# Optimization experiments

Hardware: AMD Instinct MI355X
Metric: run time of the kernel (lower is better)

The kernel has to match this reference:

```python
import jax, jax.numpy as jnp
import numpy as np

DIM = 256
HEADS = 8
DIM_HEAD = 64
HIDDEN = HEADS * DIM_HEAD
SCALE = DIM_HEAD ** -0.5


def setup_inputs() -> dict:
    key = jax.random.key(0)
    ks = jax.random.split(key, 8)
    std = 0.02
    x = jax.random.normal(ks[0], (2, DIM, 16, 64, 64), dtype=jnp.float32)
    Wq = jax.random.normal(ks[1], (HIDDEN, DIM), dtype=jnp.float32) * std
    Wk = jax.random.normal(ks[2], (HIDDEN, DIM), dtype=jnp.float32) * std
    Wv = jax.random.normal(ks[3], (HIDDEN, DIM), dtype=jnp.float32) * std
    Wg = jax.random.normal(ks[4], (HIDDEN, DIM), dtype=jnp.float32) * std
    bg = jnp.zeros((HIDDEN,), dtype=jnp.float32)
    Wo = jax.random.normal(ks[5], (DIM, HIDDEN), dtype=jnp.float32) * std
    bo = jnp.zeros((DIM,), dtype=jnp.float32)
    return {"x": x, "Wq": Wq, "Wk": Wk, "Wv": Wv, "Wg": Wg, "bg": bg, "Wo": Wo, "bo": bo}


def _proj(x, W):  # 1x1 conv, no bias: (B,C,H,W) @ (O,C) -> (B,O,H,W)
    return jnp.einsum('bchw,oc->bohw', x, W)


def reference(x, Wq, Wk, Wv, Wg, bg, Wo, bo):
    b, c, f, h, w = x.shape
    xf = x.transpose(0, 2, 1, 3, 4).reshape(b * f, c, h, w)  # (bf, c, h, w)
    q = _proj(xf, Wq)
    k = _proj(xf, Wk)
    v = _proj(xf, Wv)
    g = _proj(xf, Wg) + bg[None, :, None, None]
    # softmax over height for q, width for k (pre-reshape, as in torch)
    q = jax.nn.softmax(q, axis=-2)
    k = jax.nn.softmax(k, axis=-1)

    def to_heads(t):  # (bf, H*D, h, w) -> (bf, H, h*w, D)
        return t.reshape(b * f, HEADS, DIM_HEAD, h * w).transpose(0, 1, 3, 2)

    q, k, v, g = map(to_heads, (q, k, v, g))
    q = jax.nn.elu(q) + 1.0
    k = jax.nn.elu(k) + 1.0
    g = jax.nn.sigmoid(g)

    kv = jnp.einsum('bhnd,bhne->bhde', k, v)
    k_sum = k.sum(axis=2)                                   # (bf, H, D)
    z = 1.0 / jnp.maximum(jnp.einsum('bhnd,bhd->bhn', q, k_sum), 1e-6)
    out = jnp.einsum('bhnd,bhde->bhne', q * SCALE, kv)
    out = out * z[..., None] * g                            # (bf, H, n, D)

    out = out.transpose(0, 1, 3, 2).reshape(b * f, HIDDEN, h, w)
    out = jnp.einsum('bchw,oc->bohw', out, Wo) + bo[None, :, None, None]
    return out.reshape(b, f, c, h, w).transpose(0, 2, 1, 3, 4)
```

## Files before the change

kernel.cpp:

```cpp
#include <hip/hip_runtime.h>


typedef unsigned short u16;
typedef unsigned int u32;
typedef __bf16 bf16x8 __attribute__((ext_vector_type(8)));
typedef float f32x4 __attribute__((ext_vector_type(4)));

__device__ inline float bf2f(u16 v) { union { u32 i; float f; } u; u.i = ((u32)v) << 16; return u.f; }
__device__ inline u16 f2bf(float f) {
    union { float f; u32 i; } u; u.f = f;
    u32 r = (u.i + 0x7fffu + ((u.i >> 16) & 1u)) >> 16;
    return (u16)r;
}
__device__ inline void split2(float v, u16& h, u16& l) {
    h = f2bf(v);
    l = f2bf(v - bf2f(h));
}

__global__ void k_cvt_w(const float* __restrict__ Wq, const float* __restrict__ Wk,
                        const float* __restrict__ Wv, const float* __restrict__ Wg,
                        const float* __restrict__ Wo,
                        u16* __restrict__ Wh, u16* __restrict__ Wl,
                        u16* __restrict__ Woh, u16* __restrict__ Wol)
{
    int idx = blockIdx.x * 256 + threadIdx.x;
    if (idx < 524288) {
        int o = idx >> 8, c = idx & 255;
        int which = o >> 9, r = o & 511;
        const float* s = (which == 0) ? Wq : (which == 1) ? Wk : (which == 2) ? Wv : Wg;
        u16 h, l; split2(s[r * 256 + c], h, l);
        Wh[idx] = h; Wl[idx] = l;
    } else {
        int j = idx - 524288;
        if (j < 131072) { u16 h, l; split2(Wo[j], h, l); Woh[j] = h; Wol[j] = l; }
    }
}

__global__ __launch_bounds__(256) void k_cvt_x(const float* __restrict__ x,
                                               u16* __restrict__ xh, u16* __restrict__ xl,
                                               int c0)
{
    __shared__ __align__(16) u16 tileh[64 * 132];
    __shared__ __align__(16) u16 tilel[64 * 132];
    const int t = threadIdx.x;
    const int bfl = blockIdx.y;
    const int bfg = c0 + bfl;
    const int n0 = blockIdx.x * 128;
    const int b_ = bfg >> 4, f_ = bfg & 15;
    for (int s = 0; s < 2; ++s) {
        for (int ch2 = 0; ch2 < 2; ++ch2) {
            __syncthreads();
            for (int p = 0; p < 8; ++p) {
                int cl = p * 16 + (t >> 4);
                int c = ch2 * 128 + cl;
                const float* sp = x + (((size_t)b_ * 256 + c) * 16 + f_) * 4096
                                    + n0 + s * 64 + (t & 15) * 4;
                float4 v = *(const float4*)sp;
                float vv[4] = { v.x, v.y, v.z, v.w };
#pragma unroll
                for (int j = 0; j < 4; ++j) {
                    int nl = (t & 15) * 4 + j;
                    u16 h, l; split2(vv[j], h, l);
                    tileh[nl * 132 + cl] = h;
                    tilel[nl * 132 + cl] = l;
                }
            }
            __syncthreads();
#pragma unroll
            for (int i = 0; i < 4; ++i) {
                int flat = t + i * 256;
                int nn = flat >> 4, cc = flat & 15;
                size_t off = ((size_t)bfl * 4096 + n0 + s * 64 + nn) * 256 + ch2 * 128 + cc * 8;
                *(uint4*)(xh + off) = *(const uint4*)(tileh + nn * 132 + cc * 8);
                *(uint4*)(xl + off) = *(const uint4*)(tilel + nn * 132 + cc * 8);
            }
        }
    }
}

__global__ __launch_bounds__(256) void k_proj(
    const u16* __restrict__ Wh, const u16* __restrict__ Wl,
    const u16* __restrict__ xh, const u16* __restrict__ xl,
    const float* __restrict__ bg,
    u16* __restrict__ kh, u16* __restrict__ kl,
    u16* __restrict__ vh, u16* __restrict__ vl,
    float* __restrict__ qf, float* __restrict__ gf, int pass)
{
    __shared__ __align__(16) char smem[65536];
    u16* Ah = (u16*)smem;
    u16* Al = (u16*)(smem + 16384);
    u16* Bh = (u16*)(smem + 32768);
    u16* Bl = (u16*)(smem + 49152);
    float* Csh = (float*)smem;
    const int t = threadIdx.x;
    const int bfl = blockIdx.z;
    const int by = blockIdx.y;
    const int m0 = (pass == 0) ? (512 + by * 128)
                               : ((by < 4) ? by * 128 : 1536 + (by - 4) * 128);
    const int n0 = blockIdx.x * 128;
    const int lane = t & 63, wv = t >> 6, wm = wv >> 1, wn = wv & 1;
    f32x4 acc[4][4] = {};
    const u16* Aph = Wh + (size_t)m0 * 256;
    const u16* Apl = Wl + (size_t)m0 * 256;
    const u16* Bph = xh + ((size_t)bfl * 4096 + n0) * 256;
    const u16* Bpl = xl + ((size_t)bfl * 4096 + n0) * 256;
    const int srow = t >> 3, sci = t & 7;

    for (int kt = 0; kt < 4; ++kt) {
        const int k0 = kt * 64;
#pragma unroll
        for (int p = 0; p < 4; ++p) {
            int row = srow + p * 32;
            size_t go = (size_t)row * 256 + k0 + sci * 8;
            int sc = (sci ^ (row & 7)) * 8;
            *(uint4*)(Ah + row * 64 + sc) = *(const uint4*)(Aph + go);
            *(uint4*)(Al + row * 64 + sc) = *(const uint4*)(Apl + go);
            *(uint4*)(Bh + row * 64 + sc) = *(const uint4*)(Bph + go);
            *(uint4*)(Bl + row * 64 + sc) = *(const uint4*)(Bpl + go);
        }
        __syncthreads();
#pragma unroll
        for (int kk = 0; kk < 2; ++kk) {
            bf16x8 afh[4], afl[4], bfh[4], bfl_[4];
#pragma unroll
            for (int i = 0; i < 4; ++i) {
                int ra = wm * 64 + i * 16 + (lane & 15);
                int ca = ((kk * 4 + (lane >> 4)) ^ (ra & 7)) * 8;
                afh[i] = *(const bf16x8*)(Ah + ra * 64 + ca);
                afl[i] = *(const bf16x8*)(Al + ra * 64 + ca);
                int rb = wn * 64 + i * 16 + (lane & 15);
                int cb = ((kk * 4 + (lane >> 4)) ^ (rb & 7)) * 8;
                bfh[i] = *(const bf16x8*)(Bh + rb * 64 + cb);
                bfl_[i] = *(const bf16x8*)(Bl + rb * 64 + cb);
            }
#pragma unroll
            for (int mi = 0; mi < 4; ++mi)
#pragma unroll
                for (int ni = 0; ni < 4; ++ni) {
                    acc[mi][ni] = __builtin_amdgcn_mfma_f32_16x16x32_bf16(afh[mi], bfh[ni], acc[mi][ni], 0, 0, 0);
                    acc[mi][ni] = __builtin_amdgcn_mfma_f32_16x16x32_bf16(afh[mi], bfl_[ni], acc[mi][ni], 0, 0, 0);
                    acc[mi][ni] = __builtin_amdgcn_mfma_f32_16x16x32_bf16(afl[mi], bfh[ni], acc[mi][ni], 0, 0, 0);
                }
        }
        __syncthreads();
    }

    const int sector = m0 >> 9;
    for (int ph = 0; ph < 2; ++ph) {
        if (wn == ph) {
#pragma unroll
            for (int mi = 0; mi < 4; ++mi)
#pragma unroll
                for (int ni = 0; ni < 4; ++ni)
#pragma unroll
                    for (int r = 0; r < 4; ++r) {
                        int gr = wm * 64 + mi * 16 + (lane >> 4) * 4 + r;
                        int gcl = ni * 16 + (lane & 15);
                        Csh[gr * 69 + gcl] = acc[mi][ni][r];
                    }
        }
        __syncthreads();
        if (t < 128) {
            const float* src = Csh + t * 69;
            const int oloc = (m0 & 511) + t;
            const size_t doff = ((size_t)bfl * 512 + oloc) * 4096 + n0 + ph * 64;
            if (sector == 0) {
#pragma unroll
                for (int i = 0; i < 16; ++i) {
                    float4 o = { src[i * 4], src[i * 4 + 1], src[i * 4 + 2], src[i * 4 + 3] };
                    *(float4*)(qf + doff + i * 4) = o;
                }
            } else if (sector == 2) {
#pragma unroll
                for (int i = 0; i < 8; ++i) {
                    union { u16 h[8]; uint4 u; } ph_, pl_;
#pragma unroll
                    for (int j = 0; j < 8; ++j) split2(src[i * 8 + j], ph_.h[j], pl_.h[j]);
                    *(uint4*)(vh + doff + i * 8) = ph_.u;
                    *(uint4*)(vl + doff + i * 8) = pl_.u;
                }
            } else if (sector == 1) {
                float mx = -3.0e38f;
                for (int j = 0; j < 64; ++j) mx = fmaxf(mx, src[j]);
                float sum = 0.f;
                for (int j = 0; j < 64; ++j) sum += expf(src[j] - mx);
                float rs = 1.0f / sum;
#pragma unroll
                for (int i = 0; i < 8; ++i) {
                    union { u16 h[8]; uint4 u; } ph_, pl_;
#pragma unroll
                    for (int j = 0; j < 8; ++j) {
                        float p = expf(src[i * 8 + j] - mx) * rs;
                        split2(p, ph_.h[j], pl_.h[j]);
                    }
                    *(uint4*)(kh + doff + i * 8) = ph_.u;
                    *(uint4*)(kl + doff + i * 8) = pl_.u;
                }
            } else {
                float bgv = bg[oloc];
#pragma unroll
                for (int i = 0; i < 16; ++i) {
                    float4 o;
                    float* po = (float*)&o;
#pragma unroll
                    for (int j = 0; j < 4; ++j)
                        po[j] = 1.0f / (1.0f + expf(-(src[i * 4 + j] + bgv)));
                    *(float4*)(gf + doff + i * 4) = o;
                }
            }
        }
        __syncthreads();
    }
}

__global__ __launch_bounds__(256) void k_smq(float* __restrict__ qf)
{
    __shared__ float img[64 * 65];
    __shared__ float red[256];
    __shared__ float mxv[64];
    __shared__ float smv[64];
    const int t = threadIdx.x;
    float* base = qf + ((size_t)blockIdx.y * 512 + blockIdx.x) * 4096;
#pragma unroll
    for (int i = 0; i < 16; ++i) {
        int n = t + i * 256;
        img[(n >> 6) * 65 + (n & 63)] = base[n];
    }
    __syncthreads();
    const int part = t >> 6, wc = t & 63;
    float mx = -3.0e38f;
    for (int hh = 0; hh < 16; ++hh) mx = fmaxf(mx, img[(part * 16 + hh) * 65 + wc]);
    red[t] = mx;
    __syncthreads();
    if (t < 64) mxv[t] = fmaxf(fmaxf(red[t], red[64 + t]), fmaxf(red[128 + t], red[192 + t]));
    __syncthreads();
    float m = mxv[wc], s = 0.f;
    for (int hh = 0; hh < 16; ++hh) s += expf(img[(part * 16 + hh) * 65 + wc] - m);
    red[t] = s;
    __syncthreads();
    if (t < 64) smv[t] = red[t] + red[64 + t] + red[128 + t] + red[192 + t];
    __syncthreads();
    float rm = mxv[t & 63], rs = 1.0f / smv[t & 63];
#pragma unroll
    for (int i = 0; i < 16; ++i) {
        int n = t + i * 256;
        base[n] = expf(img[(n >> 6) * 65 + (n & 63)] - rm) * rs;
    }
}

__global__ __launch_bounds__(512) void k_kv(
    const u16* __restrict__ kh, const u16* __restrict__ kl,
    const u16* __restrict__ vh, const u16* __restrict__ vl,
    float* __restrict__ kvp, float* __restrict__ ksp)
{
    __shared__ float kvl[4096];
    __shared__ float redv[512];
    __shared__ float redk[512];
    __shared__ float vsum[64];
    const int t = threadIdx.x;
    const int qq = blockIdx.x;
    const int bh = blockIdx.y;
    const int NBH = gridDim.y;
    const size_t hb = (size_t)bh * 64 * 4096;
    const u16* bkh = kh + hb;
    const u16* bkl = kl + hb;
    const u16* bvh = vh + hb;
    const u16* bvl = vl + hb;
#pragma unroll
    for (int i = 0; i < 8; ++i) kvl[t + i * 512] = 0.f;
    __syncthreads();
    const int lane = t & 63, wv = t >> 6;
    f32x4 acc[4][4] = {};
    for (int it = 0; it < 4; ++it) {
        int n = qq * 1024 + wv * 128 + it * 32 + (lane >> 4) * 8;
        bf16x8 ah[4], al[4], bh_[4], bl_[4];
#pragma unroll
        for (int i = 0; i < 4; ++i) {
            size_t ro = (size_t)(i * 16 + (lane & 15)) * 4096 + n;
            ah[i]  = *(const bf16x8*)(bkh + ro);
            al[i]  = *(const bf16x8*)(bkl + ro);
            bh_[i] = *(const bf16x8*)(bvh + ro);
            bl_[i] = *(const bf16x8*)(bvl + ro);
        }
#pragma unroll
        for (int di = 0; di < 4; ++di)
#pragma unroll
            for (int ei = 0; ei < 4; ++ei) {
                acc[di][ei] = __builtin_amdgcn_mfma_f32_16x16x32_bf16(ah[di], bh_[ei], acc[di][ei], 0, 0, 0);
                acc[di][ei] = __builtin_amdgcn_mfma_f32_16x16x32_bf16(ah[di], bl_[ei], acc[di][ei], 0, 0, 0);
                acc[di][ei] = __builtin_amdgcn_mfma_f32_16x16x32_bf16(al[di], bh_[ei], acc[di][ei], 0, 0, 0);
            }
    }
#pragma unroll
    for (int di = 0; di < 4; ++di)
#pragma unroll
        for (int ei = 0; ei < 4; ++ei)
#pragma unroll
            for (int r = 0; r < 4; ++r) {
                int d = di * 16 + (lane >> 4) * 4 + r;
                int e = ei * 16 + (lane & 15);
                atomicAdd(&kvl[d * 64 + e], acc[di][ei][r]);
            }
    const int e = t & 63, part = t >> 6;
    float sv = 0.f, sk = 0.f;
    const size_t so = (size_t)e * 4096 + qq * 1024 + part * 128;
    for (int i = 0; i < 16; ++i) {
        union { uint4 v; u16 h[8]; } a1, a2, b1, b2;
        a1.v = *(const uint4*)(bvh + so + i * 8);
        a2.v = *(const uint4*)(bvl + so + i * 8);
        b1.v = *(const uint4*)(bkh + so + i * 8);
        b2.v = *(const uint4*)(bkl + so + i * 8);
#pragma unroll
        for (int j = 0; j < 8; ++j) {
            sv += bf2f(a1.h[j]) + bf2f(a2.h[j]);
            sk += bf2f(b1.h[j]) + bf2f(b2.h[j]);
        }
    }
    redv[t] = sv; redk[t] = sk;
    __syncthreads();
    if (t < 64) {
        float a = 0.f, b = 0.f;
#pragma unroll
        for (int p = 0; p < 8; ++p) { a += redv[p * 64 + t]; b += redk[p * 64 + t]; }
        vsum[t] = a;
        ksp[((size_t)qq * NBH + bh) * 64 + t] = 1024.0f + b;
    }
    __syncthreads();
    float* outp = kvp + ((size_t)qq * NBH + bh) * 4096;
#pragma unroll
    for (int i = 0; i < 8; ++i) {
        int idx = t + i * 512;
        outp[idx] = kvl[idx] + vsum[idx & 63];
    }
}

__global__ __launch_bounds__(256) void k_att(
    const float* __restrict__ qf, const float* __restrict__ gf,
    const float* __restrict__ kvp, const float* __restrict__ ksp,
    u16* __restrict__ atth, u16* __restrict__ attl, int NBH)
{
    __shared__ __align__(16) float sh[4352 + 64 + 64 + 16];
    float* kvl = sh;
    float* ksl = sh + 4352;
    float* csl = sh + 4416;
    float* kstp = sh + 4480;
    const int t = threadIdx.x;
    const int bh = blockIdx.z * 8 + blockIdx.y;
#pragma unroll
    for (int i = 0; i < 16; ++i) {
        int idx = t + i * 256;
        float s = 0.f;
#pragma unroll
        for (int q = 0; q < 4; ++q) s += kvp[((size_t)q * NBH + bh) * 4096 + idx];
        kvl[(idx >> 6) * 68 + (idx & 63)] = s;
    }
    if (t < 64) {
        float s = 0.f;
#pragma unroll
        for (int q = 0; q < 4; ++q) s += ksp[((size_t)q * NBH + bh) * 64 + t];
        ksl[t] = s;
    }
    __syncthreads();
    if (t < 64) {
        float s = 0.f;
        for (int d = 0; d < 64; ++d) s += kvl[d * 68 + t];
        csl[t] = s;
    }
    if (t == 64) {
        float s = 0.f;
        for (int d = 0; d < 64; ++d) s += ksl[d];
        kstp[0] = s;
    }
    __syncthreads();
    const int n = blockIdx.x * 256 + t;
    const float* qp = qf + ((size_t)bh * 64) * 4096 + n;
    f32x4 sa[16];
#pragma unroll
    for (int i = 0; i < 16; ++i) sa[i] = *(const f32x4*)&csl[i * 4];
    float sz = kstp[0];
    for (int d = 0; d < 64; ++d) {
        float pq = qp[(size_t)d * 4096];
        sz += pq * ksl[d];
        const f32x4* kr = (const f32x4*)&kvl[d * 68];
#pragma unroll
        for (int i = 0; i < 16; ++i) sa[i] += pq * kr[i];
    }
    float zz = 0.125f / fmaxf(sz, 1e-6f);
    const float* gp = gf + ((size_t)bh * 64) * 4096 + n;
    const size_t ab = (((size_t)(bh >> 3)) * 4096 + n) * 512 + (bh & 7) * 64;
#pragma unroll
    for (int eo = 0; eo < 8; ++eo) {
        union { u16 h[8]; uint4 u; } ph_, pl_;
#pragma unroll
        for (int j = 0; j < 8; ++j) {
            int e = eo * 8 + j;
            float val = sa[e >> 2][e & 3] * zz * gp[(size_t)e * 4096];
            split2(val, ph_.h[j], pl_.h[j]);
        }
        *(uint4*)(atth + ab + eo * 8) = ph_.u;
        *(uint4*)(attl + ab + eo * 8) = pl_.u;
    }
}

__global__ __launch_bounds__(256) void k_out(
    const u16* __restrict__ Woh, const u16* __restrict__ Wol,
    const u16* __restrict__ atth, const u16* __restrict__ attl,
    const float* __restrict__ bo, float* __restrict__ out, int c0)
{
    __shared__ __align__(16) u16 smem[32768];
    u16* Ah = smem;
    u16* Al = smem + 8192;
    u16* Bh = smem + 16384;
    u16* Bl = smem + 24576;
    const int t = threadIdx.x;
    const int bfl = blockIdx.z;
    const int bfg = c0 + bfl;
    const int m0 = blockIdx.y * 128;
    const int n0 = blockIdx.x * 128;
    const int lane = t & 63, wv = t >> 6, wm = wv >> 1, wn = wv & 1;
    f32x4 acc[4][4] = {};
    const u16* Aph = Woh + (size_t)m0 * 512;
    const u16* Apl = Wol + (size_t)m0 * 512;
    const u16* Bph = atth + ((size_t)bfl * 4096 + n0) * 512;
    const u16* Bpl = attl + ((size_t)bfl * 4096 + n0) * 512;
    const int srow = t >> 3, sci = t & 7;
    for (int kt = 0; kt < 8; ++kt) {
        const int k0 = kt * 64;
#pragma unroll
        for (int p = 0; p < 4; ++p) {
            int row = srow + p * 32;
            size_t go = (size_t)row * 512 + k0 + sci * 8;
            int sc = (sci ^ (row & 7)) * 8;
            *(uint4*)(Ah + row * 64 + sc) = *(const uint4*)(Aph + go);
            *(uint4*)(Al + row * 64 + sc) = *(const uint4*)(Apl + go);
            *(uint4*)(Bh + row * 64 + sc) = *(const uint4*)(Bph + go);
            *(uint4*)(Bl + row * 64 + sc) = *(const uint4*)(Bpl + go);
        }
        __syncthreads();
#pragma unroll
        for (int kk = 0; kk < 2; ++kk) {
            bf16x8 afh[4], afl[4], bfh[4], bfl_[4];
#pragma unroll
            for (int i = 0; i < 4; ++i) {
                int ra = wm * 64 + i * 16 + (lane & 15);
                int ca = ((kk * 4 + (lane >> 4)) ^ (ra & 7)) * 8;
                afh[i] = *(const bf16x8*)(Ah + ra * 64 + ca);
                afl[i] = *(const bf16x8*)(Al + ra * 64 + ca);
                int rb = wn * 64 + i * 16 + (lane & 15);
                int cb = ((kk * 4 + (lane >> 4)) ^ (rb & 7)) * 8;
                bfh[i] = *(const bf16x8*)(Bh + rb * 64 + cb);
                bfl_[i] = *(const bf16x8*)(Bl + rb * 64 + cb);
            }
#pragma unroll
            for (int mi = 0; mi < 4; ++mi)
#pragma unroll
                for (int ni = 0; ni < 4; ++ni) {
                    acc[mi][ni] = __builtin_amdgcn_mfma_f32_16x16x32_bf16(afh[mi], bfh[ni], acc[mi][ni], 0, 0, 0);
                    acc[mi][ni] = __builtin_amdgcn_mfma_f32_16x16x32_bf16(afh[mi], bfl_[ni], acc[mi][ni], 0, 0, 0);
                    acc[mi][ni] = __builtin_amdgcn_mfma_f32_16x16x32_bf16(afl[mi], bfh[ni], acc[mi][ni], 0, 0, 0);
                }
        }
        __syncthreads();
    }
    const int b_ = bfg >> 4, f_ = bfg & 15;
#pragma unroll
    for (int mi = 0; mi < 4; ++mi)
#pragma unroll
        for (int ni = 0; ni < 4; ++ni)
#pragma unroll
            for (int r = 0; r < 4; ++r) {
                int o = m0 + wm * 64 + mi * 16 + (lane >> 4) * 4 + r;
                int nn = n0 + wn * 64 + ni * 16 + (lane & 15);
                out[(((size_t)b_ * 256 + o) * 16 + f_) * 4096 + nn] = acc[mi][ni][r] + bo[o];
            }
}

extern "C" void kernel_launch(void* const* d_in, const int* in_sizes, int n_in,
                              void* d_out, int out_size, void* d_ws, size_t ws_size,
                              hipStream_t stream)
{
    const float* x  = (const float*)d_in[0];
    const float* Wq = (const float*)d_in[1];
    const float* Wk = (const float*)d_in[2];
    const float* Wv = (const float*)d_in[3];
    const float* Wg = (const float*)d_in[4];
    const float* bg = (const float*)d_in[5];
    const float* Wo = (const float*)d_in[6];
    const float* bo = (const float*)d_in[7];
    float* out = (float*)d_out;
    char* ws = (char*)d_ws;

    const size_t PER_BF = 29892608ull;
    const size_t FIXED  = 2621440ull;
    int CH = 32;
    while (CH > 1 && FIXED + (size_t)CH * PER_BF > ws_size) CH >>= 1;
    const int nch = 32 / CH;

    u16* Wh  = (u16*)(ws);
    u16* Wl  = (u16*)(ws + 1048576);
    u16* Woh = (u16*)(ws + 2097152);
    u16* Wol = (u16*)(ws + 2359296);
    char* dyn = ws + FIXED;
    u16*   xh   = (u16*)(dyn);
    u16*   xl   = (u16*)(dyn + (size_t)CH * 2097152);
    u16*   kh   = (u16*)(dyn + (size_t)CH * 4194304);
    u16*   kl   = (u16*)(dyn + (size_t)CH * 8388608);
    u16*   vh   = (u16*)(dyn + (size_t)CH * 12582912);
    u16*   vl   = (u16*)(dyn + (size_t)CH * 16777216);
    u16*   atth = (u16*)(dyn + (size_t)CH * 20971520);
    u16*   attl = (u16*)(dyn + (size_t)CH * 25165824);
    float* kvp  = (float*)(dyn + (size_t)CH * 29360128);
    float* ksp  = (float*)(dyn + (size_t)CH * 29884416);
    float* qf   = (float*)kh;
    float* gf   = (float*)vh;

    k_cvt_w<<<dim3(2560), dim3(256), 0, stream>>>(Wq, Wk, Wv, Wg, Wo, Wh, Wl, Woh, Wol);

    for (int c = 0; c < nch; ++c) {
        const int c0 = c * CH;
        k_cvt_x<<<dim3(32, CH),    dim3(256), 0, stream>>>(x, xh, xl, c0);
        k_proj <<<dim3(32, 8, CH), dim3(256), 0, stream>>>(Wh, Wl, xh, xl, bg,
                                                           kh, kl, vh, vl, qf, gf, 0);
        k_kv   <<<dim3(4, CH * 8), dim3(512), 0, stream>>>(kh, kl, vh, vl, kvp, ksp);
        k_proj <<<dim3(32, 8, CH), dim3(256), 0, stream>>>(Wh, Wl, xh, xl, bg,
                                                           kh, kl, vh, vl, qf, gf, 1);
        k_smq  <<<dim3(512, CH),   dim3(256), 0, stream>>>(qf);
        k_att  <<<dim3(16, 8, CH), dim3(256), 0, stream>>>(qf, gf, kvp, ksp, atth, attl, CH * 8);
        k_out  <<<dim3(32, 2, CH), dim3(256), 0, stream>>>(Woh, Wol, atth, attl, bo, out, c0);
    }
}
```

Baseline: 2.043 ms.

## Use direct global-to-LDS loads and restage kv reduction through shared memory

Replaces the register-staged global-to-shared tile copies in the projection and output GEMMs with global_load_lds direct-to-LDS transfers, with the swizzle moved to the source address. Rewrites k_kv to stage K and V tiles in LDS via the same mechanism, splitting the pixels over 8 blocks of 256 threads instead of 4 blocks of 512. It also folds the k and v column sums into the MFMA work by appending a ones fragment, which removes the separate summation pass that re-read K and V. k_att now reduces 8 partials plus separate v-sum partials, which adds extra workspace and some extra MFMA work in exchange for fewer global reads.

```diff
diff --git a/kernel.cpp b/kernel.cpp
--- a/kernel.cpp
+++ b/kernel.cpp
@@ -5,6 +5,12 @@
 typedef unsigned int u32;
 typedef __bf16 bf16x8 __attribute__((ext_vector_type(8)));
 typedef float f32x4 __attribute__((ext_vector_type(4)));
+
+typedef const __attribute__((address_space(1))) void* gas_t;
+typedef __attribute__((address_space(3))) void* las_t;
+__device__ __forceinline__ void gll16(const void* g, void* l) {
+    __builtin_amdgcn_global_load_lds((gas_t)g, (las_t)l, 16, 0, 0);
+}
 
 __device__ inline float bf2f(u16 v) { union { u32 i; float f; } u; u.i = ((u32)v) << 16; return u.f; }
 __device__ inline u16 f2bf(float f) {
@@ -104,19 +110,19 @@
     const u16* Apl = Wl + (size_t)m0 * 256;
     const u16* Bph = xh + ((size_t)bfl * 4096 + n0) * 256;
     const u16* Bpl = xl + ((size_t)bfl * 4096 + n0) * 256;
-    const int srow = t >> 3, sci = t & 7;
 
     for (int kt = 0; kt < 4; ++kt) {
         const int k0 = kt * 64;
 #pragma unroll
-        for (int p = 0; p < 4; ++p) {
-            int row = srow + p * 32;
-            size_t go = (size_t)row * 256 + k0 + sci * 8;
-            int sc = (sci ^ (row & 7)) * 8;
-            *(uint4*)(Ah + row * 64 + sc) = *(const uint4*)(Aph + go);
-            *(uint4*)(Al + row * 64 + sc) = *(const uint4*)(Apl + go);
-            *(uint4*)(Bh + row * 64 + sc) = *(const uint4*)(Bph + go);
-            *(uint4*)(Bl + row * 64 + sc) = *(const uint4*)(Bpl + go);
+        for (int jj = 0; jj < 4; ++jj) {
+            int s = wv * 4 + jj;
+            int row = s * 8 + (lane >> 3);
+            int csrc = (lane & 7) ^ (row & 7);
+            size_t go = (size_t)row * 256 + k0 + csrc * 8;
+            gll16(Aph + go, Ah + s * 512);
+            gll16(Apl + go, Al + s * 512);
+            gll16(Bph + go, Bh + s * 512);
+            gll16(Bpl + go, Bl + s * 512);
         }
         __syncthreads();
 #pragma unroll
@@ -248,49 +254,85 @@
     }
 }
 
-__global__ __launch_bounds__(512) void k_kv(
+__global__ __launch_bounds__(256) void k_kv(
     const u16* __restrict__ kh, const u16* __restrict__ kl,
     const u16* __restrict__ vh, const u16* __restrict__ vl,
-    float* __restrict__ kvp, float* __restrict__ ksp)
-{
-    __shared__ float kvl[4096];
-    __shared__ float redv[512];
-    __shared__ float redk[512];
-    __shared__ float vsum[64];
+    float* __restrict__ kvp, float* __restrict__ vsp, float* __restrict__ ksp)
+{
+    __shared__ __align__(16) char smem[65536];
+    u16* Kh = (u16*)smem;
+    u16* Kl = (u16*)(smem + 16384);
+    u16* Vh = (u16*)(smem + 32768);
+    u16* Vl = (u16*)(smem + 49152);
+    float* mrg = (float*)smem;
     const int t = threadIdx.x;
-    const int qq = blockIdx.x;
+    const int oct = blockIdx.x;
     const int bh = blockIdx.y;
     const int NBH = gridDim.y;
+    const int lane = t & 63, wv = t >> 6;
     const size_t hb = (size_t)bh * 64 * 4096;
-    const u16* bkh = kh + hb;
-    const u16* bkl = kl + hb;
-    const u16* bvh = vh + hb;
-    const u16* bvl = vl + hb;
-#pragma unroll
-    for (int i = 0; i < 8; ++i) kvl[t + i * 512] = 0.f;
-    __syncthreads();
-    const int lane = t & 63, wv = t >> 6;
-    f32x4 acc[4][4] = {};
-    for (int it = 0; it < 4; ++it) {
-        int n = qq * 1024 + wv * 128 + it * 32 + (lane >> 4) * 8;
+
+    f32x4 acc[5][5] = {};
+    bf16x8 ones;
+#pragma unroll
+    for (int j = 0; j < 8; ++j) ones[j] = (lane & 15) == 0 ? (__bf16)1.0f : (__bf16)0.0f;
+
+    for (int cc = 0; cc < 4; ++cc) {
+        const int pxc = oct * 512 + cc * 128;
+#pragma unroll
+        for (int jj = 0; jj < 4; ++jj) {
+            int s = wv * 4 + jj;
+            int row = s * 4 + (lane >> 4);
+            int csrc = (lane & 15) ^ (row & 7);
+            size_t go = hb + (size_t)row * 4096 + pxc + csrc * 8;
+            gll16(kh + go, Kh + s * 512);
+            gll16(kl + go, Kl + s * 512);
+            gll16(vh + go, Vh + s * 512);
+            gll16(vl + go, Vl + s * 512);
+        }
+        __syncthreads();
         bf16x8 ah[4], al[4], bh_[4], bl_[4];
 #pragma unroll
         for (int i = 0; i < 4; ++i) {
-            size_t ro = (size_t)(i * 16 + (lane & 15)) * 4096 + n;
-            ah[i]  = *(const bf16x8*)(bkh + ro);
-            al[i]  = *(const bf16x8*)(bkl + ro);
-            bh_[i] = *(const bf16x8*)(bvh + ro);
-            bl_[i] = *(const bf16x8*)(bvl + ro);
+            int ra = i * 16 + (lane & 15);
+            int kc = (wv * 4 + (lane >> 4)) ^ (ra & 7);
+            int off = ra * 128 + kc * 8;
+            ah[i]  = *(const bf16x8*)(Kh + off);
+            al[i]  = *(const bf16x8*)(Kl + off);
+            bh_[i] = *(const bf16x8*)(Vh + off);
+            bl_[i] = *(const bf16x8*)(Vl + off);
+        }
+#pragma unroll
+        for (int di = 0; di < 5; ++di) {
+            bf16x8 a = (di < 4) ? ah[di] : ones;
+#pragma unroll
+            for (int ei = 0; ei < 5; ++ei) {
+                bf16x8 b = (ei < 4) ? bh_[ei] : ones;
+                acc[di][ei] = __builtin_amdgcn_mfma_f32_16x16x32_bf16(a, b, acc[di][ei], 0, 0, 0);
+            }
+        }
+#pragma unroll
+        for (int di = 0; di < 5; ++di) {
+            bf16x8 a = (di < 4) ? ah[di] : ones;
+#pragma unroll
+            for (int ei = 0; ei < 4; ++ei)
+                acc[di][ei] = __builtin_amdgcn_mfma_f32_16x16x32_bf16(a, bl_[ei], acc[di][ei], 0, 0, 0);
         }
 #pragma unroll
         for (int di = 0; di < 4; ++di)
 #pragma unroll
-            for (int ei = 0; ei < 4; ++ei) {
-                acc[di][ei] = __builtin_amdgcn_mfma_f32_16x16x32_bf16(ah[di], bh_[ei], acc[di][ei], 0, 0, 0);
-                acc[di][ei] = __builtin_amdgcn_mfma_f32_16x16x32_bf16(ah[di], bl_[ei], acc[di][ei], 0, 0, 0);
-                acc[di][ei] = __builtin_amdgcn_mfma_f32_16x16x32_bf16(al[di], bh_[ei], acc[di][ei], 0, 0, 0);
-            }
-    }
+            for (int ei = 0; ei < 5; ++ei) {
+                bf16x8 b = (ei < 4) ? bh_[ei] : ones;
+                acc[di][ei] = __builtin_amdgcn_mfma_f32_16x16x32_bf16(al[di], b, acc[di][ei], 0, 0, 0);
+            }
+        __syncthreads();
+    }
+
+    float* kvm = mrg;
+    float* vsm = mrg + 64 * 68;
+    float* ksm = mrg + 64 * 68 + 64;
+    for (int i = t; i < 64 * 68 + 128; i += 256) mrg[i] = 0.f;
+    __syncthreads();
 #pragma unroll
     for (int di = 0; di < 4; ++di)
 #pragma unroll
@@ -299,66 +341,63 @@
             for (int r = 0; r < 4; ++r) {
                 int d = di * 16 + (lane >> 4) * 4 + r;
                 int e = ei * 16 + (lane & 15);
-                atomicAdd(&kvl[d * 64 + e], acc[di][ei][r]);
-            }
-    const int e = t & 63, part = t >> 6;
-    float sv = 0.f, sk = 0.f;
-    const size_t so = (size_t)e * 4096 + qq * 1024 + part * 128;
+                atomicAdd(&kvm[d * 68 + e], acc[di][ei][r]);
+            }
+    if (lane < 16) {
+#pragma unroll
+        for (int ei = 0; ei < 4; ++ei) atomicAdd(&vsm[ei * 16 + lane], acc[4][ei][0]);
+    }
+    if ((lane & 15) == 0) {
+#pragma unroll
+        for (int di = 0; di < 4; ++di)
+#pragma unroll
+            for (int r = 0; r < 4; ++r)
+                atomicAdd(&ksm[di * 16 + (lane >> 4) * 4 + r], acc[di][4][r]);
+    }
+    __syncthreads();
+    float* op = kvp + ((size_t)oct * NBH + bh) * 4096;
+#pragma unroll
     for (int i = 0; i < 16; ++i) {
-        union { uint4 v; u16 h[8]; } a1, a2, b1, b2;
-        a1.v = *(const uint4*)(bvh + so + i * 8);
-        a2.v = *(const uint4*)(bvl + so + i * 8);
-        b1.v = *(const uint4*)(bkh + so + i * 8);
-        b2.v = *(const uint4*)(bkl + so + i * 8);
-#pragma unroll
-        for (int j = 0; j < 8; ++j) {
-            sv += bf2f(a1.h[j]) + bf2f(a2.h[j]);
-            sk += bf2f(b1.h[j]) + bf2f(b2.h[j]);
-        }
-    }
-    redv[t] = sv; redk[t] = sk;
-    __syncthreads();
+        int idx = t + i * 256;
+        op[idx] = kvm[(idx >> 6) * 68 + (idx & 63)];
+    }
+    if (t < 64) {
+        vsp[((size_t)oct * NBH + bh) * 64 + t] = vsm[t];
+        ksp[((size_t)oct * NBH + bh) * 64 + t] = 512.0f + ksm[t];
+    }
+}
+
+__global__ __launch_bounds__(256) void k_att(
+    const float* __restrict__ qf, const float* __restrict__ gf,
+    const float* __restrict__ kvp, const float* __restrict__ vsp,
+    const float* __restrict__ ksp,
+    u16* __restrict__ atth, u16* __restrict__ attl, int NBH)
+{
+    __shared__ __align__(16) float sh[4352 + 64 + 64 + 64 + 16];
+    float* kvl = sh;
+    float* vsl = sh + 4352;
+    float* ksl = sh + 4416;
+    float* csl = sh + 4480;
+    float* kstp = sh + 4544;
+    const int t = threadIdx.x;
+    const int bh = blockIdx.z * 8 + blockIdx.y;
     if (t < 64) {
         float a = 0.f, b = 0.f;
 #pragma unroll
-        for (int p = 0; p < 8; ++p) { a += redv[p * 64 + t]; b += redk[p * 64 + t]; }
-        vsum[t] = a;
-        ksp[((size_t)qq * NBH + bh) * 64 + t] = 1024.0f + b;
-    }
-    __syncthreads();
-    float* outp = kvp + ((size_t)qq * NBH + bh) * 4096;
-#pragma unroll
-    for (int i = 0; i < 8; ++i) {
-        int idx = t + i * 512;
-        outp[idx] = kvl[idx] + vsum[idx & 63];
-    }
-}
-
-__global__ __launch_bounds__(256) void k_att(
-    const float* __restrict__ qf, const float* __restrict__ gf,
-    const float* __restrict__ kvp, const float* __restrict__ ksp,
-    u16* __restrict__ atth, u16* __restrict__ attl, int NBH)
-{
-    __shared__ __align__(16) float sh[4352 + 64 + 64 + 16];
-    float* kvl = sh;
-    float* ksl = sh + 4352;
-    float* csl = sh + 4416;
-    float* kstp = sh + 4480;
-    const int t = threadIdx.x;
-    const int bh = blockIdx.z * 8 + blockIdx.y;
+        for (int o = 0; o < 8; ++o) {
+            a += vsp[((size_t)o * NBH + bh) * 64 + t];
+            b += ksp[((size_t)o * NBH + bh) * 64 + t];
+        }
+        vsl[t] = a; ksl[t] = b;
+    }
+    __syncthreads();
 #pragma unroll
     for (int i = 0; i < 16; ++i) {
         int idx = t + i * 256;
-        float s = 0.f;
-#pragma unroll
-        for (int q = 0; q < 4; ++q) s += kvp[((size_t)q * NBH + bh) * 4096 + idx];
+        float s = vsl[idx & 63];
+#pragma unroll
+        for (int o = 0; o < 8; ++o) s += kvp[((size_t)o * NBH + bh) * 4096 + idx];
         kvl[(idx >> 6) * 68 + (idx & 63)] = s;
-    }
-    if (t < 64) {
-        float s = 0.f;
-#pragma unroll
-        for (int q = 0; q < 4; ++q) s += ksp[((size_t)q * NBH + bh) * 64 + t];
-        ksl[t] = s;
     }
     __syncthreads();
     if (t < 64) {
@@ -423,18 +462,18 @@
     const u16* Apl = Wol + (size_t)m0 * 512;
     const u16* Bph = atth + ((size_t)bfl * 4096 + n0) * 512;
     const u16* Bpl = attl + ((size_t)bfl * 4096 + n0) * 512;
-    const int srow = t >> 3, sci = t & 7;
     for (int kt = 0; kt < 8; ++kt) {
         const int k0 = kt * 64;
 #pragma unroll
-        for (int p = 0; p < 4; ++p) {
-            int row = srow + p * 32;
-            size_t go = (size_t)row * 512 + k0 + sci * 8;
-            int sc = (sci ^ (row & 7)) * 8;
-            *(uint4*)(Ah + row * 64 + sc) = *(const uint4*)(Aph + go);
-            *(uint4*)(Al + row * 64 + sc) = *(const uint4*)(Apl + go);
-            *(uint4*)(Bh + row * 64 + sc) = *(const uint4*)(Bph + go);
-            *(uint4*)(Bl + row * 64 + sc) = *(const uint4*)(Bpl + go);
+        for (int jj = 0; jj < 4; ++jj) {
+            int s = wv * 4 + jj;
+            int row = s * 8 + (lane >> 3);
+            int csrc = (lane & 7) ^ (row & 7);
+            size_t go = (size_t)row * 512 + k0 + csrc * 8;
+            gll16(Aph + go, Ah + s * 512);
+            gll16(Apl + go, Al + s * 512);
+            gll16(Bph + go, Bh + s * 512);
+            gll16(Bpl + go, Bl + s * 512);
         }
         __syncthreads();
 #pragma unroll
@@ -490,7 +529,7 @@
     float* out = (float*)d_out;
     char* ws = (char*)d_ws;
 
-    const size_t PER_BF = 29892608ull;
+    const size_t PER_BF = 30441472ull;
     const size_t FIXED  = 2621440ull;
     int CH = 32;
     while (CH > 1 && FIXED + (size_t)CH * PER_BF > ws_size) CH >>= 1;
@@ -510,7 +549,8 @@
     u16*   atth = (u16*)(dyn + (size_t)CH * 20971520);
     u16*   attl = (u16*)(dyn + (size_t)CH * 25165824);
     float* kvp  = (float*)(dyn + (size_t)CH * 29360128);
-    float* ksp  = (float*)(dyn + (size_t)CH * 29884416);
+    float* vsp  = (float*)(dyn + (size_t)CH * 30408704);
+    float* ksp  = (float*)(dyn + (size_t)CH * 30425088);
     float* qf   = (float*)kh;
     float* gf   = (float*)vh;
 
@@ -521,11 +561,11 @@
         k_cvt_x<<<dim3(32, CH),    dim3(256), 0, stream>>>(x, xh, xl, c0);
         k_proj <<<dim3(32, 8, CH), dim3(256), 0, stream>>>(Wh, Wl, xh, xl, bg,
                                                            kh, kl, vh, vl, qf, gf, 0);
-        k_kv   <<<dim3(4, CH * 8), dim3(512), 0, stream>>>(kh, kl, vh, vl, kvp, ksp);
+        k_kv   <<<dim3(8, CH * 8), dim3(256), 0, stream>>>(kh, kl, vh, vl, kvp, vsp, ksp);
         k_proj <<<dim3(32, 8, CH), dim3(256), 0, stream>>>(Wh, Wl, xh, xl, bg,
                                                            kh, kl, vh, vl, qf, gf, 1);
         k_smq  <<<dim3(512, CH),   dim3(256), 0, stream>>>(qf);
-        k_att  <<<dim3(16, 8, CH), dim3(256), 0, stream>>>(qf, gf, kvp, ksp, atth, attl, CH * 8);
+        k_att  <<<dim3(16, 8, CH), dim3(256), 0, stream>>>(qf, gf, kvp, vsp, ksp, atth, attl, CH * 8);
         k_out  <<<dim3(32, 2, CH), dim3(256), 0, stream>>>(Woh, Wol, atth, attl, bo, out, c0);
     }
 }
```

Result: faster. 1.898 ms (-7.1%).
